# Kernel tuning notes

Measured on AMD Instinct MI355X. Metric: run time of the kernel, lower is better.

The kernel has to match this reference:

```python
import jax, jax.numpy as jnp
import numpy as np
import math

D_MODEL = 128      # embedding_dim
D_STATE = 64
D_CONV = 4
NHEADS = 4         # d_inner / headdim (Mamba2 default headdim=64)
HEADDIM = 64
D_INNER = 256      # expand * d_model
CONV_DIM = 384     # d_inner + 2*ngroups*d_state (ngroups=1)
D_IN_PROJ = 644    # 2*d_inner + 2*ngroups*d_state + nheads
NLAYERS = 2
INPUT_DIM = 768
EPS = 1e-5


def setup_inputs() -> dict:
    key = jax.random.key(0)
    ks = jax.random.split(key, 20)
    rn = lambda k, s, sd=0.02: jax.random.normal(k, s, jnp.float32) * sd
    return {
        "x": jax.random.normal(ks[0], (16, 1024, INPUT_DIM), jnp.float32),
        "fc1_W": rn(ks[1], (INPUT_DIM, D_MODEL)),
        "fc1_b": jnp.zeros((D_MODEL,), jnp.float32),
        "ln_w": jnp.ones((NLAYERS, D_MODEL), jnp.float32),
        "ln_b": jnp.zeros((NLAYERS, D_MODEL), jnp.float32),
        "in_W": rn(ks[2], (NLAYERS, D_MODEL, D_IN_PROJ)),
        "conv_w": rn(ks[3], (NLAYERS, D_CONV, CONV_DIM), 0.1),
        "conv_b": jnp.zeros((NLAYERS, CONV_DIM), jnp.float32),
        "dt_bias": rn(ks[4], (NLAYERS, NHEADS), 0.5),
        "A_log": jnp.log(jax.random.uniform(ks[5], (NLAYERS, NHEADS), jnp.float32, 1.0, 16.0)),
        "Dp": jnp.ones((NLAYERS, NHEADS), jnp.float32),
        "rms_w": jnp.ones((NLAYERS, D_INNER), jnp.float32),
        "out_W": rn(ks[6], (NLAYERS, D_INNER, D_MODEL)),
        "fc2_W1": rn(ks[7], (D_MODEL, D_MODEL)),
        "fc2_b1": jnp.zeros((D_MODEL,), jnp.float32),
        "fc2_W2": rn(ks[8], (D_MODEL, 6)),
        "fc2_b2": jnp.zeros((6,), jnp.float32),
    }


def _pos_embedding(L):
    pos = jnp.arange(L, dtype=jnp.float32)[:, None]                       # (L,1)
    div = jnp.exp(jnp.arange(0, D_MODEL, 2, dtype=jnp.float32) * (-math.log(10000.0) / D_MODEL))
    pe = jnp.zeros((L, D_MODEL), jnp.float32)
    pe = pe.at[:, 0::2].set(jnp.sin(pos * div))
    pe = pe.at[:, 1::2].set(jnp.cos(pos * div))
    return pe[None]                                                        # (1,L,D)


def _layernorm(x, w, b):
    mu = jnp.mean(x, -1, keepdims=True)
    var = jnp.mean(jnp.square(x - mu), -1, keepdims=True)
    return (x - mu) * jax.lax.rsqrt(var + EPS) * w + b


def _mamba2(u, in_W, conv_w, conv_b, dt_bias, A_log, Dp, rms_w, out_W):
    b, l, _ = u.shape
    zxbcdt = u @ in_W                                                      # (b,l,644)
    z = zxbcdt[..., :D_INNER]
    xBC = zxbcdt[..., D_INNER:D_INNER + CONV_DIM]
    dt = jax.nn.softplus(zxbcdt[..., D_INNER + CONV_DIM:] + dt_bias)       # (b,l,h)
    # causal depthwise conv1d (width 4) + SiLU
    xp = jnp.pad(xBC, ((0, 0), (D_CONV - 1, 0), (0, 0)))
    xc = conv_b
    for k in range(D_CONV):
        xc = xc + conv_w[k] * xp[:, k:k + l, :]
    xc = jax.nn.silu(xc)                                                   # (b,l,384)
    xh = xc[..., :D_INNER].reshape(b, l, NHEADS, HEADDIM)                  # (b,l,h,p)
    B = xc[..., D_INNER:D_INNER + D_STATE]                                 # (b,l,n)
    C = xc[..., D_INNER + D_STATE:]                                        # (b,l,n)
    A = -jnp.exp(A_log)                                                    # (h,)
    dA = jnp.exp(dt * A)                                                   # (b,l,h)
    dtx = dt[..., None] * xh                                               # (b,l,h,p)

    def step(h, inp):
        dA_t, dtx_t, B_t, C_t = inp                                        # (b,h),(b,h,p),(b,n),(b,n)
        h = dA_t[..., None, None] * h + dtx_t[..., None] * B_t[:, None, None, :]
        y = jnp.einsum('bhpn,bn->bhp', h, C_t)
        return h, y

    h0 = jnp.zeros((b, NHEADS, HEADDIM, D_STATE), u.dtype)
    _, ys = jax.lax.scan(step, h0, (dA.transpose(1, 0, 2), dtx.transpose(1, 0, 2, 3),
                                    B.transpose(1, 0, 2), C.transpose(1, 0, 2)))
    y = ys.transpose(1, 0, 2, 3) + Dp[None, None, :, None] * xh            # (b,l,h,p)
    y = y.reshape(b, l, D_INNER)
    # gated RMSNorm: rmsnorm(y * silu(z)) * weight
    y = y * jax.nn.silu(z)
    y = y * jax.lax.rsqrt(jnp.mean(jnp.square(y), -1, keepdims=True) + EPS) * rms_w
    return y @ out_W


def reference(x, fc1_W, fc1_b, ln_w, ln_b, in_W, conv_w, conv_b, dt_bias,
              A_log, Dp, rms_w, out_W, fc2_W1, fc2_b1, fc2_W2, fc2_b2):
    h = x @ fc1_W + fc1_b                                                  # (b,l,128)
    h = h + _pos_embedding(h.shape[1])
    for i in range(NLAYERS):
        res = h
        hn = _layernorm(h, ln_w[i], ln_b[i])
        h = _mamba2(hn, in_W[i], conv_w[i], conv_b[i], dt_bias[i],
                    A_log[i], Dp[i], rms_w[i], out_W[i]) + res
        # dropout: identity in eval mode
    h = jax.nn.leaky_relu(h @ fc2_W1 + fc2_b1, negative_slope=0.1)
    return h @ fc2_W2 + fc2_b2                                             # (b,l,6)
```

## Files before the change

kernel.cpp:

```cpp
#include <hip/hip_runtime.h>
#include <hip/hip_bf16.h>

#define BATCH 16
#define SEQ 1024
#define NROWS (BATCH*SEQ)
#define IN_DIM 768
#define DM 128
#define DIP 644
#define DI 256
#define CDIM 384
#define DST 64
#define NH 4
#define HD 64
#define CHUNK 64
#define NCHUNK (SEQ/CHUNK)

#define WB_FC1   0
#define WB_IN    98304
#define WB_OUT   263168
#define WB_FC2   328704
#define WB_TOTAL 345088

typedef __attribute__((ext_vector_type(8))) short short8;
typedef __attribute__((ext_vector_type(4))) float float4v;

__device__ __forceinline__ short f2b(float f) {
    unsigned u = __builtin_bit_cast(unsigned, f);
    u += 0x7fffu + ((u >> 16) & 1u);
    return (short)(u >> 16);
}
__device__ __forceinline__ float s2f(short s) {
    unsigned u = ((unsigned)(unsigned short)s) << 16;
    return __builtin_bit_cast(float, u);
}
__device__ __forceinline__ short8 pack8f(float4 a, float4 b) {
    short8 r;
    r[0] = f2b(a.x); r[1] = f2b(a.y); r[2] = f2b(a.z); r[3] = f2b(a.w);
    r[4] = f2b(b.x); r[5] = f2b(b.y); r[6] = f2b(b.z); r[7] = f2b(b.w);
    return r;
}
__device__ __forceinline__ float silu(float a) { return a / (1.f + expf(-a)); }

__global__ void prep_weights(const float* __restrict__ fc1_W, const float* __restrict__ in_W,
                             const float* __restrict__ out_W, const float* __restrict__ fc2_W1,
                             short* __restrict__ wb) {
    int idx = blockIdx.x * 256 + threadIdx.x;
    if (idx < 98304) {
        int n = idx / 768, k = idx % 768;
        wb[WB_FC1 + idx] = f2b(fc1_W[k * 128 + n]);
        return;
    }
    idx -= 98304;
    if (idx < 2 * 82432) {
        int l = idx / 82432, r = idx % 82432;
        int n = r / 128, k = r % 128;
        wb[WB_IN + idx] = f2b(in_W[(size_t)l * 82432 + k * 644 + n]);
        return;
    }
    idx -= 164864;
    if (idx < 2 * 32768) {
        int l = idx / 32768, r = idx % 32768;
        int n = r / 256, k = r % 256;
        wb[WB_OUT + idx] = f2b(out_W[(size_t)l * 32768 + k * 128 + n]);
        return;
    }
    idx -= 65536;
    if (idx < 16384) {
        int n = idx / 128, k = idx % 128;
        wb[WB_FC2 + idx] = f2b(fc2_W1[k * 128 + n]);
    }
}

#define GEMM_PROLOGUE() \
    int tid = threadIdx.x; \
    int lane = tid & 63; \
    int m = lane & 15; \
    int kq = (lane >> 4) * 8; \
    int w = tid >> 6; \
    int mrow = (w & 3) * 16; \
    int ngrp = w >> 2; \
    int a_off = (mrow + m) * 72 + kq; \
    int b_off = (ngrp * 64 + m) * 72 + kq; \
    int ar = tid >> 3; \
    int ak = (tid & 7) * 8; \
    (void)ar; (void)ak; \
    float4v acc[4]; \
    acc[0] = (float4v)0.f; acc[1] = (float4v)0.f; acc[2] = (float4v)0.f; acc[3] = (float4v)0.f;

#define GEMM_COMPUTE_TILE() \
    { \
        short8 a0 = *reinterpret_cast<const short8*>(&As[a_off]); \
        short8 a1 = *reinterpret_cast<const short8*>(&As[a_off + 32]); \
        _Pragma("unroll") \
        for (int nt = 0; nt < 4; nt++) { \
            short8 b0 = *reinterpret_cast<const short8*>(&Bt[b_off + nt * 16 * 72]); \
            short8 b1 = *reinterpret_cast<const short8*>(&Bt[b_off + nt * 16 * 72 + 32]); \
            acc[nt] = __builtin_amdgcn_mfma_f32_16x16x32_bf16(a0, b0, acc[nt], 0, 0, 0); \
            acc[nt] = __builtin_amdgcn_mfma_f32_16x16x32_bf16(a1, b1, acc[nt], 0, 0, 0); \
        } \
    }

#define GEMM_STAGE_B(wtptr, LDB, k0) \
    _Pragma("unroll") \
    for (int i = 0; i < 2; i++) { \
        int idx = tid + i * 512; \
        int n = idx >> 3, kk = (idx & 7) * 8; \
        *reinterpret_cast<short8*>(&Bt[n * 72 + kk]) = \
            *reinterpret_cast<const short8*>(&wtptr[n * (LDB) + (k0) + kk]); \
    }

__global__ __launch_bounds__(512) void fc1_mfma(const float* __restrict__ x,
                                                const short* __restrict__ wt,
                                                const float* __restrict__ bias,
                                                const float* __restrict__ lnw0,
                                                const float* __restrict__ lnb0,
                                                float* __restrict__ h,
                                                short* __restrict__ hnb) {
    __shared__ short As[32 * 72];
    __shared__ short Bt[128 * 72];
    __shared__ float ps1[32][4], ps2[32][4];
    int tid = threadIdx.x;
    int lane = tid & 63;
    int m = lane & 15;
    int quad = lane >> 4;
    int kq = quad * 8;
    int w = tid >> 6;
    int mrow = (w & 1) * 16;
    int ngrp = w >> 1;
    int ar = tid >> 4;
    int ac = (tid & 15) * 4;
    int row0 = blockIdx.x * 32;
    float4v acc[2];
    acc[0] = (float4v)0.f; acc[1] = (float4v)0.f;
    for (int kt = 0; kt < 12; kt++) {
        int k0 = kt * 64;
        if (kt) __syncthreads();
        {
            const float* src = x + (size_t)(row0 + ar) * IN_DIM + k0 + ac;
            float4 v = *(const float4*)src;
            short4 pv;
            pv.x = f2b(v.x); pv.y = f2b(v.y); pv.z = f2b(v.z); pv.w = f2b(v.w);
            *reinterpret_cast<short4*>(&As[ar * 72 + ac]) = pv;
        }
        GEMM_STAGE_B(wt, 768, k0);
        __syncthreads();
        short8 a0 = *reinterpret_cast<const short8*>(&As[(mrow + m) * 72 + kq]);
        short8 a1 = *reinterpret_cast<const short8*>(&As[(mrow + m) * 72 + kq + 32]);
        #pragma unroll
        for (int nt = 0; nt < 2; nt++) {
            int bo = (ngrp * 32 + nt * 16 + m) * 72 + kq;
            short8 b0 = *reinterpret_cast<const short8*>(&Bt[bo]);
            short8 b1 = *reinterpret_cast<const short8*>(&Bt[bo + 32]);
            acc[nt] = __builtin_amdgcn_mfma_f32_16x16x32_bf16(a0, b0, acc[nt], 0, 0, 0);
            acc[nt] = __builtin_amdgcn_mfma_f32_16x16x32_bf16(a1, b1, acc[nt], 0, 0, 0);
        }
    }
    float val[2][4];
    float s1r[4] = {0.f,0.f,0.f,0.f}, s2r[4] = {0.f,0.f,0.f,0.f};
    #pragma unroll
    for (int nt = 0; nt < 2; nt++) {
        int col = ngrp * 32 + nt * 16 + m;
        float bv = bias[col];
        float div = expf(-(float)(col & ~1) * 0.071955784f);
        #pragma unroll
        for (int r = 0; r < 4; r++) {
            int row = row0 + mrow + quad * 4 + r;
            int t = row & (SEQ - 1);
            float arg = (float)t * div;
            float pe = (col & 1) ? cosf(arg) : sinf(arg);
            float v = acc[nt][r] + bv + pe;
            val[nt][r] = v;
            s1r[r] += v; s2r[r] += v * v;
        }
    }
    #pragma unroll
    for (int o = 1; o < 16; o <<= 1) {
        #pragma unroll
        for (int r = 0; r < 4; r++) {
            s1r[r] += __shfl_xor(s1r[r], o);
            s2r[r] += __shfl_xor(s2r[r], o);
        }
    }
    if (m == 0) {
        #pragma unroll
        for (int r = 0; r < 4; r++) {
            ps1[mrow + quad * 4 + r][ngrp] = s1r[r];
            ps2[mrow + quad * 4 + r][ngrp] = s2r[r];
        }
    }
    __syncthreads();
    #pragma unroll
    for (int r = 0; r < 4; r++) {
        int rl = mrow + quad * 4 + r;
        float s1 = ps1[rl][0] + ps1[rl][1] + ps1[rl][2] + ps1[rl][3];
        float s2 = ps2[rl][0] + ps2[rl][1] + ps2[rl][2] + ps2[rl][3];
        float mu = s1 * (1.f / 128.f);
        float rs = rsqrtf(s2 * (1.f / 128.f) - mu * mu + 1e-5f);
        int row = row0 + rl;
        #pragma unroll
        for (int nt = 0; nt < 2; nt++) {
            int col = ngrp * 32 + nt * 16 + m;
            float v = val[nt][r];
            h[(size_t)row * DM + col] = v;
            hnb[(size_t)row * DM + col] = f2b((v - mu) * rs * lnw0[col] + lnb0[col]);
        }
    }
}

__global__ __launch_bounds__(512) void inproj_mfma(const short* __restrict__ hnb,
                                                   const short* __restrict__ wb,
                                                   short* __restrict__ zb,
                                                   short* __restrict__ xbc,
                                                   float* __restrict__ dtb,
                                                   const float* __restrict__ dt_bias, int layer) {
    __shared__ short As[64 * 72];
    __shared__ short Bt[128 * 72];
    GEMM_PROLOGUE();
    int row0 = blockIdx.x * 64;
    int ncol0 = blockIdx.y * 128;
    const short* wt = wb + WB_IN + (size_t)layer * 82432;
    for (int kt = 0; kt < 2; kt++) {
        int k0 = kt * 64;
        if (kt) __syncthreads();
        *reinterpret_cast<short8*>(&As[ar * 72 + ak]) =
            *reinterpret_cast<const short8*>(&hnb[(size_t)(row0 + ar) * DM + k0 + ak]);
        #pragma unroll
        for (int i = 0; i < 2; i++) {
            int idx = tid + i * 512;
            int n = idx >> 3, kk = (idx & 7) * 8;
            int col = ncol0 + n;
            short8 bv = (short8)0;
            if (col < DIP) bv = *reinterpret_cast<const short8*>(&wt[col * 128 + k0 + kk]);
            *reinterpret_cast<short8*>(&Bt[n * 72 + kk]) = bv;
        }
        __syncthreads();
        GEMM_COMPUTE_TILE();
    }
    #pragma unroll
    for (int nt = 0; nt < 4; nt++) {
        int col = ncol0 + ngrp * 64 + nt * 16 + m;
        if (col < DI) {
            #pragma unroll
            for (int r = 0; r < 4; r++) {
                int row = row0 + mrow + (lane >> 4) * 4 + r;
                zb[(size_t)row * DI + col] = f2b(acc[nt][r]);
            }
        } else if (col < DI + CDIM) {
            #pragma unroll
            for (int r = 0; r < 4; r++) {
                int row = row0 + mrow + (lane >> 4) * 4 + r;
                xbc[(size_t)row * CDIM + (col - DI)] = f2b(acc[nt][r]);
            }
        } else if (col < DIP) {
            int hh = col - DI - CDIM;
            float db = dt_bias[layer * NH + hh];
            #pragma unroll
            for (int r = 0; r < 4; r++) {
                int row = row0 + mrow + (lane >> 4) * 4 + r;
                float raw = acc[nt][r] + db;
                float dt = (raw > 20.f) ? raw : log1pf(expf(raw));
                dtb[(size_t)row * NH + hh] = dt;
            }
        }
    }
}

__global__ void conv_kernel(const short* __restrict__ xbc,
                            const float* __restrict__ convw, const float* __restrict__ convb,
                            short* __restrict__ xcb, int layer) {
    int c = threadIdx.x;
    int row0 = blockIdx.x * 4;
    int l0 = row0 & (SEQ - 1);
    const float* cw = convw + (size_t)layer * 4 * CDIM;
    float w0 = cw[c], w1 = cw[CDIM + c], w2 = cw[2 * CDIM + c], w3 = cw[3 * CDIM + c];
    float bb = convb[layer * CDIM + c];
    float v[7];
    #pragma unroll
    for (int i = 0; i < 7; i++) {
        int rr = row0 + i - 3;
        v[i] = (l0 + i - 3 >= 0) ? s2f(xbc[(size_t)rr * CDIM + c]) : 0.f;
    }
    #pragma unroll
    for (int j = 0; j < 4; j++) {
        float acc = bb + w0 * v[j] + w1 * v[j + 1] + w2 * v[j + 2] + w3 * v[j + 3];
        xcb[(size_t)(row0 + j) * CDIM + c] = f2b(silu(acc));
    }
}

__global__ __launch_bounds__(256) void chunk_state_mfma(const short* __restrict__ xcb,
                                                        const float* __restrict__ dtb,
                                                        const float* __restrict__ A_log,
                                                        short* __restrict__ Slocb,
                                                        float* __restrict__ decay, int layer) {
    __shared__ short XTw[64 * 72];
    __shared__ short BT[64 * 72];
    __shared__ float wst[64];
    int bid = blockIdx.x;
    int c  = bid & (NCHUNK - 1);
    int hh = (bid >> 4) & (NH - 1);
    int b  = bid >> 6;
    int tid = threadIdx.x;
    int row0 = b * SEQ + c * CHUNK;
    float A = -expf(A_log[layer * NH + hh]);

    if (tid < CHUNK) {
        float dtv = dtb[(size_t)(row0 + tid) * NH + hh];
        float l = dtv * A;
        #pragma unroll
        for (int o = 1; o < 64; o <<= 1) { float v = __shfl_up(l, o); if (tid >= o) l += v; }
        float Ltot = __shfl(l, 63);
        wst[tid] = expf(Ltot - l) * dtv;
        if (tid == 63) decay[bid] = expf(Ltot);
    }
    __syncthreads();
    {
        int p = tid & 63;
        int tb0 = tid >> 6;
        #pragma unroll
        for (int i = 0; i < 2; i++) {
            int t0 = (tb0 + i * 4) * 8;
            short8 xv, bv;
            #pragma unroll
            for (int j = 0; j < 8; j++) {
                int t = t0 + j;
                const short* xr = xcb + (size_t)(row0 + t) * CDIM;
                xv[j] = f2b(s2f(xr[hh * HD + p]) * wst[t]);
                bv[j] = xr[DI + p];
            }
            *reinterpret_cast<short8*>(&XTw[p * 72 + t0]) = xv;
            *reinterpret_cast<short8*>(&BT[p * 72 + t0]) = bv;
        }
    }
    __syncthreads();

    int lane = tid & 63;
    int m = lane & 15;
    int kq = (lane >> 4) * 8;
    int w = tid >> 6;
    int a_off = (w * 16 + m) * 72 + kq;
    float4v acc[4];
    acc[0] = (float4v)0.f; acc[1] = (float4v)0.f; acc[2] = (float4v)0.f; acc[3] = (float4v)0.f;
    short8 a0 = *reinterpret_cast<const short8*>(&XTw[a_off]);
    short8 a1 = *reinterpret_cast<const short8*>(&XTw[a_off + 32]);
    #pragma unroll
    for (int nt = 0; nt < 4; nt++) {
        int bo = (nt * 16 + m) * 72 + kq;
        short8 b0 = *reinterpret_cast<const short8*>(&BT[bo]);
        short8 b1 = *reinterpret_cast<const short8*>(&BT[bo + 32]);
        acc[nt] = __builtin_amdgcn_mfma_f32_16x16x32_bf16(a0, b0, acc[nt], 0, 0, 0);
        acc[nt] = __builtin_amdgcn_mfma_f32_16x16x32_bf16(a1, b1, acc[nt], 0, 0, 0);
    }
    short* Sp = Slocb + (size_t)bid * (HD * DST);
    int tq = (lane >> 4) * 4;
    #pragma unroll
    for (int nt = 0; nt < 4; nt++) {
        #pragma unroll
        for (int r = 0; r < 4; r++) {
            int p = w * 16 + tq + r;
            int n = nt * 16 + m;
            Sp[p * DST + n] = f2b(acc[nt][r]);
        }
    }
}

__global__ void chunk_scan_kernel(const short* __restrict__ Slocb, const float* __restrict__ decay,
                                  short* __restrict__ hstrb) {
    int bh = blockIdx.x;
    int tid = threadIdx.x;
    float hreg[16];
    #pragma unroll
    for (int k = 0; k < 16; k++) hreg[k] = 0.f;
    for (int c = 0; c < NCHUNK; c++) {
        size_t base = ((size_t)bh * NCHUNK + c) * (HD * DST) + tid * 16;
        float d = decay[bh * NCHUNK + c];
        short8 s0 = *reinterpret_cast<const short8*>(&Slocb[base]);
        short8 s1 = *reinterpret_cast<const short8*>(&Slocb[base + 8]);
        short8 h0, h1;
        #pragma unroll
        for (int k = 0; k < 8; k++) { h0[k] = f2b(hreg[k]); h1[k] = f2b(hreg[8 + k]); }
        *reinterpret_cast<short8*>(&hstrb[base]) = h0;
        *reinterpret_cast<short8*>(&hstrb[base + 8]) = h1;
        #pragma unroll
        for (int k = 0; k < 8; k++) {
            hreg[k]     = d * hreg[k]     + s2f(s0[k]);
            hreg[8 + k] = d * hreg[8 + k] + s2f(s1[k]);
        }
    }
}

__global__ __launch_bounds__(256) void chunk_out_mfma(const short* __restrict__ xcb,
                                                      const float* __restrict__ dtb,
                                                      const float* __restrict__ A_log,
                                                      const float* __restrict__ Dpw,
                                                      const short* __restrict__ hstrb,
                                                      short* __restrict__ ybb, int layer) {
    __shared__ short Cb[64 * 72];
    __shared__ short Bb[64 * 72];
    __shared__ short XT[64 * 72];
    __shared__ short HT[64 * 72];
    __shared__ float Ls[64], dts[64];
    int bid = blockIdx.x;
    int c  = bid & (NCHUNK - 1);
    int hh = (bid >> 4) & (NH - 1);
    int b  = bid >> 6;
    int tid = threadIdx.x;
    int row0 = b * SEQ + c * CHUNK;
    float A = -expf(A_log[layer * NH + hh]);
    float Dph = Dpw[layer * NH + hh];

    if (tid < CHUNK) {
        float dtv = dtb[(size_t)(row0 + tid) * NH + hh];
        float l = dtv * A;
        #pragma unroll
        for (int o = 1; o < 64; o <<= 1) { float v = __shfl_up(l, o); if (tid >= o) l += v; }
        Ls[tid] = l;
        dts[tid] = dtv;
    }
    {
        int p = tid & 63;
        int tb0 = tid >> 6;
        #pragma unroll
        for (int i = 0; i < 2; i++) {
            int t0 = (tb0 + i * 4) * 8;
            short8 xv;
            #pragma unroll
            for (int j = 0; j < 8; j++)
                xv[j] = xcb[(size_t)(row0 + t0 + j) * CDIM + hh * HD + p];
            *reinterpret_cast<short8*>(&XT[p * 72 + t0]) = xv;
        }
    }
    #pragma unroll
    for (int i = 0; i < 2; i++) {
        int idx = tid + i * 256;
        int t = idx >> 3, cb = (idx & 7) * 8;
        const short* xr = xcb + (size_t)(row0 + t) * CDIM;
        *reinterpret_cast<short8*>(&Bb[t * 72 + cb]) =
            *reinterpret_cast<const short8*>(&xr[DI + cb]);
        *reinterpret_cast<short8*>(&Cb[t * 72 + cb]) =
            *reinterpret_cast<const short8*>(&xr[DI + DST + cb]);
    }
    {
        const short* hs = hstrb + (size_t)bid * (HD * DST);
        #pragma unroll
        for (int i = 0; i < 2; i++) {
            int idx = tid + i * 256;
            int pp = idx >> 3, nb = (idx & 7) * 8;
            *reinterpret_cast<short8*>(&HT[pp * 72 + nb]) =
                *reinterpret_cast<const short8*>(&hs[pp * 64 + nb]);
        }
    }
    __syncthreads();

    int lane = tid & 63;
    int m = lane & 15;
    int kq = (lane >> 4) * 8;
    int w = tid >> 6;
    int tq = (lane >> 4) * 4;
    int a_off = (w * 16 + m) * 72 + kq;

    short8 ca0 = *reinterpret_cast<const short8*>(&Cb[a_off]);
    short8 ca1 = *reinterpret_cast<const short8*>(&Cb[a_off + 32]);

    float4v g[4], ir[4];
    #pragma unroll
    for (int i = 0; i < 4; i++) { g[i] = (float4v)0.f; ir[i] = (float4v)0.f; }
    #pragma unroll
    for (int st = 0; st < 4; st++) {
        int bo = (st * 16 + m) * 72 + kq;
        short8 b0 = *reinterpret_cast<const short8*>(&Bb[bo]);
        short8 b1 = *reinterpret_cast<const short8*>(&Bb[bo + 32]);
        g[st] = __builtin_amdgcn_mfma_f32_16x16x32_bf16(ca0, b0, g[st], 0, 0, 0);
        g[st] = __builtin_amdgcn_mfma_f32_16x16x32_bf16(ca1, b1, g[st], 0, 0, 0);
        short8 h0 = *reinterpret_cast<const short8*>(&HT[bo]);
        short8 h1 = *reinterpret_cast<const short8*>(&HT[bo + 32]);
        ir[st] = __builtin_amdgcn_mfma_f32_16x16x32_bf16(ca0, h0, ir[st], 0, 0, 0);
        ir[st] = __builtin_amdgcn_mfma_f32_16x16x32_bf16(ca1, h1, ir[st], 0, 0, 0);
    }
    __syncthreads();
    #pragma unroll
    for (int st = 0; st < 4; st++) {
        #pragma unroll
        for (int r = 0; r < 4; r++) {
            int t = w * 16 + tq + r;
            int s = st * 16 + m;
            float mv = 0.f;
            if (s <= t) mv = g[st][r] * expf(Ls[t] - Ls[s]) * dts[s];
            Bb[t * 72 + s] = f2b(mv);
        }
    }
    __syncthreads();
    float4v yi[4];
    #pragma unroll
    for (int i = 0; i < 4; i++) yi[i] = (float4v)0.f;
    short8 ma0 = *reinterpret_cast<const short8*>(&Bb[a_off]);
    short8 ma1 = *reinterpret_cast<const short8*>(&Bb[a_off + 32]);
    #pragma unroll
    for (int pt = 0; pt < 4; pt++) {
        int bo = (pt * 16 + m) * 72 + kq;
        short8 x0 = *reinterpret_cast<const short8*>(&XT[bo]);
        short8 x1 = *reinterpret_cast<const short8*>(&XT[bo + 32]);
        yi[pt] = __builtin_amdgcn_mfma_f32_16x16x32_bf16(ma0, x0, yi[pt], 0, 0, 0);
        yi[pt] = __builtin_amdgcn_mfma_f32_16x16x32_bf16(ma1, x1, yi[pt], 0, 0, 0);
    }
    #pragma unroll
    for (int r = 0; r < 4; r++) {
        int t = w * 16 + tq + r;
        float et = expf(Ls[t]);
        short* yr = ybb + (size_t)(row0 + t) * DI + hh * HD;
        #pragma unroll
        for (int pt = 0; pt < 4; pt++) {
            int p = pt * 16 + m;
            float xv = s2f(XT[p * 72 + t]);
            yr[p] = f2b(yi[pt][r] + et * ir[pt][r] + Dph * xv);
        }
    }
}

__global__ __launch_bounds__(512) void outproj_gate_mfma(const short* __restrict__ ybb,
                                                         const short* __restrict__ zb,
                                                         const float* __restrict__ rmsw,
                                                         const short* __restrict__ wb,
                                                         const float* __restrict__ lnw2,
                                                         const float* __restrict__ lnb2,
                                                         float* __restrict__ h,
                                                         short* __restrict__ hnb,
                                                         int layer, int write_hn) {
    __shared__ __align__(16) char smem[64 * 133 * 4];
    short* As = (short*)smem;
    short* Bt = (short*)(smem + 64 * 72 * 2);
    float* hs = (float*)smem;
    __shared__ float rs_s[64];
    GEMM_PROLOGUE();
    int row0 = blockIdx.x * 64;
    const short* wt = wb + WB_OUT + (size_t)layer * 32768;
    {
        int r = tid >> 3, j = tid & 7;
        const short8* yr = (const short8*)(ybb + (size_t)(row0 + r) * DI + j * 32);
        const short8* zr = (const short8*)(zb + (size_t)(row0 + r) * DI + j * 32);
        float s2 = 0.f;
        #pragma unroll
        for (int i = 0; i < 4; i++) {
            short8 yv = yr[i];
            short8 zv = zr[i];
            #pragma unroll
            for (int q = 0; q < 8; q++) {
                float v = s2f(yv[q]) * silu(s2f(zv[q]));
                s2 += v * v;
            }
        }
        #pragma unroll
        for (int o = 1; o < 8; o <<= 1) s2 += __shfl_xor(s2, o);
        if (j == 0) rs_s[r] = rsqrtf(s2 * (1.f / 256.f) + 1e-5f);
    }
    __syncthreads();
    for (int kt = 0; kt < 4; kt++) {
        int k0 = kt * 64;
        if (kt) __syncthreads();
        {
            int k = k0 + ak;
            short8 yv = *(const short8*)(ybb + (size_t)(row0 + ar) * DI + k);
            short8 zv = *(const short8*)(zb + (size_t)(row0 + ar) * DI + k);
            float4 w0 = *(const float4*)(rmsw + layer * DI + k);
            float4 w1 = *(const float4*)(rmsw + layer * DI + k + 4);
            float rs = rs_s[ar];
            short8 av;
            av[0] = f2b(s2f(yv[0]) * silu(s2f(zv[0])) * rs * w0.x);
            av[1] = f2b(s2f(yv[1]) * silu(s2f(zv[1])) * rs * w0.y);
            av[2] = f2b(s2f(yv[2]) * silu(s2f(zv[2])) * rs * w0.z);
            av[3] = f2b(s2f(yv[3]) * silu(s2f(zv[3])) * rs * w0.w);
            av[4] = f2b(s2f(yv[4]) * silu(s2f(zv[4])) * rs * w1.x);
            av[5] = f2b(s2f(yv[5]) * silu(s2f(zv[5])) * rs * w1.y);
            av[6] = f2b(s2f(yv[6]) * silu(s2f(zv[6])) * rs * w1.z);
            av[7] = f2b(s2f(yv[7]) * silu(s2f(zv[7])) * rs * w1.w);
            *reinterpret_cast<short8*>(&As[ar * 72 + ak]) = av;
        }
        GEMM_STAGE_B(wt, 256, k0);
        __syncthreads();
        GEMM_COMPUTE_TILE();
    }
    __syncthreads();
    #pragma unroll
    for (int nt = 0; nt < 4; nt++) {
        int col = ngrp * 64 + nt * 16 + m;
        #pragma unroll
        for (int r = 0; r < 4; r++) {
            int rr = mrow + (lane >> 4) * 4 + r;
            hs[rr * 133 + col] = acc[nt][r];
        }
    }
    __syncthreads();
    {
        int r = tid >> 3, j = tid & 7;
        int row = row0 + r;
        float* hdst = h + (size_t)row * DM + j * 16;
        float vals[16]; float s1 = 0.f, s2 = 0.f;
        #pragma unroll
        for (int i = 0; i < 4; i++) {
            float4 ho = *(const float4*)(hdst + i * 4);
            float v0 = ho.x + hs[r * 133 + j * 16 + i * 4];
            float v1 = ho.y + hs[r * 133 + j * 16 + i * 4 + 1];
            float v2 = ho.z + hs[r * 133 + j * 16 + i * 4 + 2];
            float v3 = ho.w + hs[r * 133 + j * 16 + i * 4 + 3];
            vals[i*4] = v0; vals[i*4+1] = v1; vals[i*4+2] = v2; vals[i*4+3] = v3;
            s1 += v0 + v1 + v2 + v3;
            s2 += v0*v0 + v1*v1 + v2*v2 + v3*v3;
        }
        #pragma unroll
        for (int o = 1; o < 8; o <<= 1) { s1 += __shfl_xor(s1, o); s2 += __shfl_xor(s2, o); }
        #pragma unroll
        for (int i = 0; i < 4; i++)
            *(float4*)(hdst + i * 4) = make_float4(vals[i*4], vals[i*4+1], vals[i*4+2], vals[i*4+3]);
        if (write_hn) {
            float mu = s1 * (1.f / 128.f);
            float rs = rsqrtf(s2 * (1.f / 128.f) - mu * mu + 1e-5f);
            const float* lw = lnw2 + j * 16;
            const float* lb = lnb2 + j * 16;
            short8 a0, a1;
            #pragma unroll
            for (int i = 0; i < 8; i++) {
                a0[i] = f2b((vals[i] - mu) * rs * lw[i] + lb[i]);
                a1[i] = f2b((vals[8 + i] - mu) * rs * lw[8 + i] + lb[8 + i]);
            }
            short* hndst = hnb + (size_t)row * DM + j * 16;
            *reinterpret_cast<short8*>(hndst) = a0;
            *reinterpret_cast<short8*>(hndst + 8) = a1;
        }
    }
}

__global__ __launch_bounds__(512) void fc2ab_mfma(const float* __restrict__ h,
                                                  const short* __restrict__ wb,
                                                  const float* __restrict__ b1,
                                                  const float* __restrict__ W2,
                                                  const float* __restrict__ b2,
                                                  float* __restrict__ out) {
    __shared__ short As[64 * 72];
    __shared__ short Bt[128 * 72];
    __shared__ float h2s[64][132];
    __shared__ float w2s[768];
    GEMM_PROLOGUE();
    int row0 = blockIdx.x * 64;
    const short* wt = wb + WB_FC2;
    for (int i = tid; i < 768; i += 512) w2s[i] = W2[i];
    for (int kt = 0; kt < 2; kt++) {
        int k0 = kt * 64;
        if (kt) __syncthreads();
        {
            const float* src = h + (size_t)(row0 + ar) * DM + k0 + ak;
            float4 v0 = *(const float4*)src;
            float4 v1 = *(const float4*)(src + 4);
            *reinterpret_cast<short8*>(&As[ar * 72 + ak]) = pack8f(v0, v1);
        }
        GEMM_STAGE_B(wt, 128, k0);
        __syncthreads();
        GEMM_COMPUTE_TILE();
    }
    #pragma unroll
    for (int nt = 0; nt < 4; nt++) {
        int col = ngrp * 64 + nt * 16 + m;
        float bv = b1[col];
        #pragma unroll
        for (int r = 0; r < 4; r++) {
            int rr = mrow + (lane >> 4) * 4 + r;
            float o = acc[nt][r] + bv;
            h2s[rr][col] = (o > 0.f) ? o : 0.1f * o;
        }
    }
    __syncthreads();
    if (tid < 384) {
        int r = tid / 6, cc = tid % 6;
        float acc2 = b2[cc];
        #pragma unroll 16
        for (int k = 0; k < 128; k++) acc2 += h2s[r][k] * w2s[k * 6 + cc];
        out[(size_t)(row0 + r) * 6 + cc] = acc2;
    }
}

extern "C" void kernel_launch(void* const* d_in, const int* in_sizes, int n_in,
                              void* d_out, int out_size, void* d_ws, size_t ws_size,
                              hipStream_t stream) {
    const float* x       = (const float*)d_in[0];
    const float* fc1_W   = (const float*)d_in[1];
    const float* fc1_b   = (const float*)d_in[2];
    const float* ln_w    = (const float*)d_in[3];
    const float* ln_b    = (const float*)d_in[4];
    const float* in_W    = (const float*)d_in[5];
    const float* conv_w  = (const float*)d_in[6];
    const float* conv_b  = (const float*)d_in[7];
    const float* dt_bias = (const float*)d_in[8];
    const float* A_log   = (const float*)d_in[9];
    const float* Dp      = (const float*)d_in[10];
    const float* rms_w   = (const float*)d_in[11];
    const float* out_W   = (const float*)d_in[12];
    const float* fc2_W1  = (const float*)d_in[13];
    const float* fc2_b1  = (const float*)d_in[14];
    const float* fc2_W2  = (const float*)d_in[15];
    const float* fc2_b2  = (const float*)d_in[16];
    float* out = (float*)d_out;

    float* ws = (float*)d_ws;
    float* h     = ws;
    float* dtb   = h     + (size_t)NROWS * DM;
    float* decay = dtb   + (size_t)NROWS * NH;
    short* sbase = (short*)(decay + 1024);
    short* hnb   = sbase;
    short* zb    = hnb   + (size_t)NROWS * DM;
    short* xbc   = zb    + (size_t)NROWS * DI;
    short* xcb   = xbc   + (size_t)NROWS * CDIM;
    short* ybb   = xcb   + (size_t)NROWS * CDIM;
    short* Slocb = ybb   + (size_t)NROWS * DI;
    short* hstrb = Slocb + (size_t)BATCH*NH*NCHUNK*HD*DST;
    short* wb    = hstrb + (size_t)BATCH*NH*NCHUNK*HD*DST;

    prep_weights<<<1348, 256, 0, stream>>>(fc1_W, in_W, out_W, fc2_W1, wb);
    fc1_mfma<<<NROWS / 32, 512, 0, stream>>>(x, wb + WB_FC1, fc1_b, ln_w, ln_b, h, hnb);

    for (int layer = 0; layer < 2; layer++) {
        inproj_mfma<<<dim3(NROWS / 64, 6), 512, 0, stream>>>(hnb, wb, zb, xbc, dtb,
                                                             dt_bias, layer);
        conv_kernel<<<NROWS / 4, CDIM, 0, stream>>>(xbc, conv_w, conv_b, xcb, layer);
        chunk_state_mfma<<<BATCH*NH*NCHUNK, 256, 0, stream>>>(xcb, dtb, A_log, Slocb, decay, layer);
        chunk_scan_kernel<<<BATCH*NH, 256, 0, stream>>>(Slocb, decay, hstrb);
        chunk_out_mfma<<<BATCH*NH*NCHUNK, 256, 0, stream>>>(xcb, dtb, A_log, Dp, hstrb, ybb, layer);
        outproj_gate_mfma<<<NROWS / 64, 512, 0, stream>>>(ybb, zb, rms_w, wb,
                                                          ln_w + DM, ln_b + DM, h, hnb,
                                                          layer, layer == 0 ? 1 : 0);
    }

    fc2ab_mfma<<<NROWS / 64, 512, 0, stream>>>(h, wb, fc2_b1, fc2_W2, fc2_b2, out);
}
```

Measured before the change: 261.4 us.

## Fuse inter-chunk state scan into chunk output kernel, recomputing prefix per block

Removes the separate chunk_scan kernel and the hstrb buffer. Each chunk_out block now builds its incoming state by replaying the decay/accumulate recurrence over all preceding chunk states, then writes it straight into shared memory. This drops one launch and a global write/read round trip of the states. In exchange the recurrence work and Slocb reads grow quadratically in chunk count, averaging about 7.5 chunk reads per block, and later chunks carry more load than earlier ones.

```diff
diff --git a/kernel.cpp b/kernel.cpp
--- a/kernel.cpp
+++ b/kernel.cpp
@@ -363,36 +363,12 @@
     }
 }
 
-__global__ void chunk_scan_kernel(const short* __restrict__ Slocb, const float* __restrict__ decay,
-                                  short* __restrict__ hstrb) {
-    int bh = blockIdx.x;
-    int tid = threadIdx.x;
-    float hreg[16];
-    #pragma unroll
-    for (int k = 0; k < 16; k++) hreg[k] = 0.f;
-    for (int c = 0; c < NCHUNK; c++) {
-        size_t base = ((size_t)bh * NCHUNK + c) * (HD * DST) + tid * 16;
-        float d = decay[bh * NCHUNK + c];
-        short8 s0 = *reinterpret_cast<const short8*>(&Slocb[base]);
-        short8 s1 = *reinterpret_cast<const short8*>(&Slocb[base + 8]);
-        short8 h0, h1;
-        #pragma unroll
-        for (int k = 0; k < 8; k++) { h0[k] = f2b(hreg[k]); h1[k] = f2b(hreg[8 + k]); }
-        *reinterpret_cast<short8*>(&hstrb[base]) = h0;
-        *reinterpret_cast<short8*>(&hstrb[base + 8]) = h1;
-        #pragma unroll
-        for (int k = 0; k < 8; k++) {
-            hreg[k]     = d * hreg[k]     + s2f(s0[k]);
-            hreg[8 + k] = d * hreg[8 + k] + s2f(s1[k]);
-        }
-    }
-}
-
 __global__ __launch_bounds__(256) void chunk_out_mfma(const short* __restrict__ xcb,
                                                       const float* __restrict__ dtb,
                                                       const float* __restrict__ A_log,
                                                       const float* __restrict__ Dpw,
-                                                      const short* __restrict__ hstrb,
+                                                      const short* __restrict__ Slocb,
+                                                      const float* __restrict__ decay,
                                                       short* __restrict__ ybb, int layer) {
     __shared__ short Cb[64 * 72];
     __shared__ short Bb[64 * 72];
@@ -405,6 +381,7 @@
     int b  = bid >> 6;
     int tid = threadIdx.x;
     int row0 = b * SEQ + c * CHUNK;
+    int bh0 = bid & ~(NCHUNK - 1);
     float A = -expf(A_log[layer * NH + hh]);
     float Dph = Dpw[layer * NH + hh];
 
@@ -415,6 +392,29 @@
         for (int o = 1; o < 64; o <<= 1) { float v = __shfl_up(l, o); if (tid >= o) l += v; }
         Ls[tid] = l;
         dts[tid] = dtv;
+    }
+    {
+        float hreg[16];
+        #pragma unroll
+        for (int k = 0; k < 16; k++) hreg[k] = 0.f;
+        for (int j = 0; j < c; j++) {
+            float d = decay[bh0 + j];
+            const short* Sp = Slocb + (size_t)(bh0 + j) * (HD * DST) + tid * 16;
+            short8 s0 = *reinterpret_cast<const short8*>(Sp);
+            short8 s1 = *reinterpret_cast<const short8*>(Sp + 8);
+            #pragma unroll
+            for (int k = 0; k < 8; k++) {
+                hreg[k]     = d * hreg[k]     + s2f(s0[k]);
+                hreg[8 + k] = d * hreg[8 + k] + s2f(s1[k]);
+            }
+        }
+        int p = tid >> 2;
+        int n0 = (tid & 3) * 16;
+        short8 h0, h1;
+        #pragma unroll
+        for (int k = 0; k < 8; k++) { h0[k] = f2b(hreg[k]); h1[k] = f2b(hreg[8 + k]); }
+        *reinterpret_cast<short8*>(&HT[p * 72 + n0]) = h0;
+        *reinterpret_cast<short8*>(&HT[p * 72 + n0 + 8]) = h1;
     }
     {
         int p = tid & 63;
@@ -438,16 +438,6 @@
             *reinterpret_cast<const short8*>(&xr[DI + cb]);
         *reinterpret_cast<short8*>(&Cb[t * 72 + cb]) =
             *reinterpret_cast<const short8*>(&xr[DI + DST + cb]);
-    }
-    {
-        const short* hs = hstrb + (size_t)bid * (HD * DST);
-        #pragma unroll
-        for (int i = 0; i < 2; i++) {
-            int idx = tid + i * 256;
-            int pp = idx >> 3, nb = (idx & 7) * 8;
-            *reinterpret_cast<short8*>(&HT[pp * 72 + nb]) =
-                *reinterpret_cast<const short8*>(&hs[pp * 64 + nb]);
-        }
     }
     __syncthreads();
 
@@ -709,8 +699,7 @@
     short* xcb   = xbc   + (size_t)NROWS * CDIM;
     short* ybb   = xcb   + (size_t)NROWS * CDIM;
     short* Slocb = ybb   + (size_t)NROWS * DI;
-    short* hstrb = Slocb + (size_t)BATCH*NH*NCHUNK*HD*DST;
-    short* wb    = hstrb + (size_t)BATCH*NH*NCHUNK*HD*DST;
+    short* wb    = Slocb + (size_t)BATCH*NH*NCHUNK*HD*DST;
 
     prep_weights<<<1348, 256, 0, stream>>>(fc1_W, in_W, out_W, fc2_W1, wb);
     fc1_mfma<<<NROWS / 32, 512, 0, stream>>>(x, wb + WB_FC1, fc1_b, ln_w, ln_b, h, hnb);
@@ -720,8 +709,8 @@
                                                              dt_bias, layer);
         conv_kernel<<<NROWS / 4, CDIM, 0, stream>>>(xbc, conv_w, conv_b, xcb, layer);
         chunk_state_mfma<<<BATCH*NH*NCHUNK, 256, 0, stream>>>(xcb, dtb, A_log, Slocb, decay, layer);
-        chunk_scan_kernel<<<BATCH*NH, 256, 0, stream>>>(Slocb, decay, hstrb);
-        chunk_out_mfma<<<BATCH*NH*NCHUNK, 256, 0, stream>>>(xcb, dtb, A_log, Dp, hstrb, ybb, layer);
+        chunk_out_mfma<<<BATCH*NH*NCHUNK, 256, 0, stream>>>(xcb, dtb, A_log, Dp, Slocb, decay,
+                                                            ybb, layer);
         outproj_gate_mfma<<<NROWS / 64, 512, 0, stream>>>(ybb, zb, rms_w, wb,
                                                           ln_w + DM, ln_b + DM, h, hnb,
                                                           layer, layer == 0 ? 1 : 0);
```

Measured after the change: 260.0 us. Within noise of the previous version (-0.6%).
